# Optimization experiments

Hardware: AMD Instinct MI355X
Metric: run time of the kernel (lower is better)

## Reference

```python
import jax, jax.numpy as jnp
import numpy as np
import math

W = 64  # window_size == chunk_size == 64


def _windows(x, w):
    """x: [b, t, ...] -> [b, nb, 2w, ...]: for block j, concat(block j-1, block j).
    Block -1 is zero padding; its validity is handled by the attention mask."""
    b, t = x.shape[0], x.shape[1]
    nb = t // w
    pad = [(0, 0), (w, 0)] + [(0, 0)] * (x.ndim - 2)
    xp = jnp.pad(x, pad)                                   # [b, t+w, ...]
    xb = xp.reshape((b, nb + 1, w) + x.shape[2:])          # [b, nb+1, w, ...]
    return jnp.concatenate([xb[:, :-1], xb[:, 1:]], axis=2)  # [b, nb, 2w, ...]


def setup_inputs() -> dict:
    key = jax.random.key(0)
    k1, k2, k3 = jax.random.split(key, 3)
    b, t, h, d = 4, 4096, 16, 64
    return {
        "q": jax.random.normal(k1, (b, t, h, d), dtype=jnp.float32),
        "k": jax.random.normal(k2, (b, t, h, d), dtype=jnp.float32),
        "v": jax.random.normal(k3, (b, t, h, d), dtype=jnp.float32),
        "attn_mask": jnp.ones((b, t), dtype=jnp.int32),
    }


def reference(q, k, v, attn_mask):
    b, t, h, d = q.shape
    nb = t // W
    scale = 1.0 / math.sqrt(d)

    qb = q.reshape(b, nb, W, h, d)
    kw = _windows(k, W)                         # [b, nb, 2W, h, d]
    vw = _windows(v, W)                         # [b, nb, 2W, h, d]
    mw = _windows(attn_mask.astype(bool), W)    # [b, nb, 2W]

    # query local index i attends to key local index m iff 0 <= (i+W-m) < W
    i = jnp.arange(W)[:, None]
    m = jnp.arange(2 * W)[None, :]
    diff = i + W - m
    band = (diff >= 0) & (diff < W)             # [W, 2W]

    valid = band[None, None] & mw[:, :, None, :]          # [b, nb, W, 2W]

    scores = jnp.einsum('bnqhd,bnkhd->bnhqk', qb, kw) * scale  # [b,nb,h,W,2W]
    scores = jnp.where(valid[:, :, None], scores, jnp.float32(-1e9))
    attn = jax.nn.softmax(scores, axis=-1)
    attn = attn * valid[:, :, None].astype(attn.dtype)

    qm = attn_mask.astype(q.dtype).reshape(b, nb, W)      # query validity
    attn = attn * qm[:, :, None, :, None]

    out = jnp.einsum('bnhqk,bnkhd->bnqhd', attn, vw)      # [b,nb,W,h,d]
    out = out * qm[:, :, :, None, None]
    return out.reshape(b, t, h, d)
```

## Files before the change

kernel.cpp:

```cpp
#include <hip/hip_runtime.h>
#include <hip/hip_bf16.h>


#define TT 4096
#define HH 16
#define DD 64
#define WW 64
#define NBLK (TT / WW)

typedef __attribute__((ext_vector_type(8))) short bf16x8;
typedef __attribute__((ext_vector_type(4))) float f32x4;

static __device__ __forceinline__ ushort f2bf(float x) {
    return __builtin_bit_cast(unsigned short, __float2bfloat16(x));
}
static __device__ __forceinline__ uint pack2(float a, float b) {
    return (uint)f2bf(a) | ((uint)f2bf(b) << 16);
}

__global__ __launch_bounds__(256, 3)
void lca_fwd(const float* __restrict__ q, const float* __restrict__ k,
             const float* __restrict__ v, const int* __restrict__ am,
             float* __restrict__ out)
{
    const int jb = blockIdx.x;
    const int hi = blockIdx.y;
    const int bi = blockIdx.z;

    __shared__ union {
        struct { ushort Q[64][72]; ushort K[128][72]; } qk;
        ushort P[64][136];
    } u;
    __shared__ ushort sVt[64][136];
    __shared__ int    sKv[128];
    __shared__ int    sQv[64];

    const int tid = threadIdx.x;
    const size_t rowstride = (size_t)HH * DD;
    const size_t qbase = ((size_t)(bi * TT + jb * WW) * HH + hi) * DD;
    const long  kstart = (long)jb * WW - WW;

    if (tid < 128) {
        long tok = kstart + tid;
        sKv[tid] = (tok >= 0) && (am[(size_t)bi * TT + tok] != 0);
    } else if (tid < 192) {
        int r = tid - 128;
        sQv[r] = (am[(size_t)bi * TT + jb * WW + r] != 0);
    }

    float4 fq[4], fk[8], fv[8];
    #pragma unroll
    for (int p = 0; p < 4; ++p) {
        int idx = p * 256 + tid;
        int row = idx >> 4, c4 = (idx & 15) * 4;
        fq[p] = *(const float4*)(q + qbase + (size_t)row * rowstride + c4);
    }
    if (jb > 0) {
        #pragma unroll
        for (int p = 0; p < 8; ++p) {
            int idx = p * 256 + tid;
            int row = idx >> 4, c4 = (idx & 15) * 4;
            fk[p] = *(const float4*)(k + ((size_t)(bi * TT + kstart + row) * HH + hi) * DD + c4);
        }
        #pragma unroll
        for (int p = 0; p < 8; ++p) {
            int idx = p * 256 + tid;
            int row = idx >> 4, c4 = (idx & 15) * 4;
            fv[p] = *(const float4*)(v + ((size_t)(bi * TT + kstart + row) * HH + hi) * DD + c4);
        }
    } else {
        #pragma unroll
        for (int p = 0; p < 8; ++p) {
            float4 z = make_float4(0.f, 0.f, 0.f, 0.f);
            if (p >= 4) {
                int idx = p * 256 + tid;
                int row = idx >> 4, c4 = (idx & 15) * 4;
                z = *(const float4*)(k + ((size_t)(bi * TT + (row - 64)) * HH + hi) * DD + c4);
            }
            fk[p] = z;
        }
        #pragma unroll
        for (int p = 0; p < 8; ++p) {
            float4 z = make_float4(0.f, 0.f, 0.f, 0.f);
            if (p >= 4) {
                int idx = p * 256 + tid;
                int row = idx >> 4, c4 = (idx & 15) * 4;
                z = *(const float4*)(v + ((size_t)(bi * TT + (row - 64)) * HH + hi) * DD + c4);
            }
            fv[p] = z;
        }
    }

    #pragma unroll
    for (int p = 0; p < 4; ++p) {
        int idx = p * 256 + tid;
        int row = idx >> 4, c4 = (idx & 15) * 4;
        uint2 w; w.x = pack2(fq[p].x, fq[p].y); w.y = pack2(fq[p].z, fq[p].w);
        *(uint2*)(&u.qk.Q[row][c4]) = w;
    }
    #pragma unroll
    for (int p = 0; p < 8; ++p) {
        int idx = p * 256 + tid;
        int row = idx >> 4, c4 = (idx & 15) * 4;
        uint2 w; w.x = pack2(fk[p].x, fk[p].y); w.y = pack2(fk[p].z, fk[p].w);
        *(uint2*)(&u.qk.K[row][c4]) = w;
    }
    #pragma unroll
    for (int p = 0; p < 8; ++p) {
        int idx = p * 256 + tid;
        int row = idx >> 4, c4 = (idx & 15) * 4;
        sVt[c4 + 0][row] = f2bf(fv[p].x);
        sVt[c4 + 1][row] = f2bf(fv[p].y);
        sVt[c4 + 2][row] = f2bf(fv[p].z);
        sVt[c4 + 3][row] = f2bf(fv[p].w);
    }
    __syncthreads();

    const int wv = tid >> 6, lane = tid & 63;
    const int quad = lane >> 4, l15 = lane & 15;
    const int r0 = 16 * wv + quad * 4;

    bf16x8 aq0 = *(const bf16x8*)(&u.qk.Q[16 * wv + l15][quad * 8]);
    bf16x8 aq1 = *(const bf16x8*)(&u.qk.Q[16 * wv + l15][32 + quad * 8]);

    f32x4 acc[8];
    #pragma unroll
    for (int kt = 0; kt < 8; ++kt) {
        f32x4 a = {0.f, 0.f, 0.f, 0.f};
        bf16x8 b0 = *(const bf16x8*)(&u.qk.K[16 * kt + l15][quad * 8]);
        bf16x8 b1 = *(const bf16x8*)(&u.qk.K[16 * kt + l15][32 + quad * 8]);
        a = __builtin_amdgcn_mfma_f32_16x16x32_bf16(aq0, b0, a, 0, 0, 0);
        a = __builtin_amdgcn_mfma_f32_16x16x32_bf16(aq1, b1, a, 0, 0, 0);
        acc[kt] = a;
    }
    __syncthreads();

    const float NEG = -1.0e9f;
    float rmax[4] = {NEG, NEG, NEG, NEG};
    #pragma unroll
    for (int kt = 0; kt < 8; ++kt) {
        int c = 16 * kt + l15;
        int kvc = sKv[c];
        #pragma unroll
        for (int reg = 0; reg < 4; ++reg) {
            int r = r0 + reg;
            bool valid = (c > r) && (c <= r + WW) && kvc;
            float s = valid ? acc[kt][reg] : NEG;
            acc[kt][reg] = s;
            rmax[reg] = fmaxf(rmax[reg], s);
        }
    }
    #pragma unroll
    for (int reg = 0; reg < 4; ++reg) {
        #pragma unroll
        for (int m = 1; m <= 8; m <<= 1)
            rmax[reg] = fmaxf(rmax[reg], __shfl_xor(rmax[reg], m, 64));
    }

    const float CEXP = 0.125f * 1.44269504088896f;
    float rsum[4] = {0.f, 0.f, 0.f, 0.f};
    #pragma unroll
    for (int kt = 0; kt < 8; ++kt) {
        int c = 16 * kt + l15;
        #pragma unroll
        for (int reg = 0; reg < 4; ++reg) {
            float s = acc[kt][reg];
            float pex = (s > -1.0e8f) ? exp2f((s - rmax[reg]) * CEXP) : 0.f;
            rsum[reg] += pex;
            u.P[r0 + reg][c] = f2bf(pex);
        }
    }
    float rden[4];
    #pragma unroll
    for (int reg = 0; reg < 4; ++reg) {
        #pragma unroll
        for (int m = 1; m <= 8; m <<= 1)
            rsum[reg] += __shfl_xor(rsum[reg], m, 64);
        rden[reg] = (rsum[reg] > 0.f ? 1.f / rsum[reg] : 0.f)
                    * (float)sQv[r0 + reg];
    }

    bf16x8 ap[4];
    #pragma unroll
    for (int kc = 0; kc < 4; ++kc)
        ap[kc] = *(const bf16x8*)(&u.P[16 * wv + l15][kc * 32 + quad * 8]);

    #pragma unroll
    for (int nt = 0; nt < 4; ++nt) {
        f32x4 a = {0.f, 0.f, 0.f, 0.f};
        #pragma unroll
        for (int kc = 0; kc < 4; ++kc) {
            bf16x8 bv = *(const bf16x8*)(&sVt[16 * nt + l15][kc * 32 + quad * 8]);
            a = __builtin_amdgcn_mfma_f32_16x16x32_bf16(ap[kc], bv, a, 0, 0, 0);
        }
        #pragma unroll
        for (int reg = 0; reg < 4; ++reg)
            out[qbase + (size_t)(r0 + reg) * rowstride + 16 * nt + l15]
                = a[reg] * rden[reg];
    }
}

extern "C" void kernel_launch(void* const* d_in, const int* in_sizes, int n_in,
                              void* d_out, int out_size, void* d_ws, size_t ws_size,
                              hipStream_t stream) {
    const float* q  = (const float*)d_in[0];
    const float* k  = (const float*)d_in[1];
    const float* v  = (const float*)d_in[2];
    const int*   am = (const int*)d_in[3];
    float* out = (float*)d_out;

    const int b = in_sizes[3] / TT;
    dim3 grid(NBLK, HH, b);
    dim3 block(256);
    lca_fwd<<<grid, block, 0, stream>>>(q, k, v, am, out);
}
```

Before: 228.1 us.

## Swizzle LDS layouts, load Q directly to registers, ballot masks, reorder blocks

Replaces the padded shared-memory arrays with XOR-swizzled unpadded buffers for K, P and transposed V. Q is now loaded straight into MFMA operand registers instead of going through LDS. The attention-mask validity arrays are replaced by wavefront ballots. LDS use drops enough to allow raising the occupancy hint from 3 to 5. Block indices are also permuted so neighbouring chunks run on different workgroups, which may change L2 reuse of the overlapping K/V windows.

```diff
diff --git a/kernel.cpp b/kernel.cpp
--- a/kernel.cpp
+++ b/kernel.cpp
@@ -18,43 +18,34 @@
     return (uint)f2bf(a) | ((uint)f2bf(b) << 16);
 }
 
-__global__ __launch_bounds__(256, 3)
+__global__ __launch_bounds__(256, 5)
 void lca_fwd(const float* __restrict__ q, const float* __restrict__ k,
              const float* __restrict__ v, const int* __restrict__ am,
              float* __restrict__ out)
 {
-    const int jb = blockIdx.x;
+    const int jb = ((blockIdx.x & 7) << 3) | (blockIdx.x >> 3);
     const int hi = blockIdx.y;
     const int bi = blockIdx.z;
 
-    __shared__ union {
-        struct { ushort Q[64][72]; ushort K[128][72]; } qk;
-        ushort P[64][136];
-    } u;
-    __shared__ ushort sVt[64][136];
-    __shared__ int    sKv[128];
-    __shared__ int    sQv[64];
-
-    const int tid = threadIdx.x;
+    __shared__ ushort sKP[8192];
+    __shared__ ushort sVt[8192];
+
+    const int tid  = threadIdx.x;
+    const int wv   = tid >> 6, lane = tid & 63;
+    const int quad = lane >> 4, l15 = lane & 15;
+
     const size_t rowstride = (size_t)HH * DD;
     const size_t qbase = ((size_t)(bi * TT + jb * WW) * HH + hi) * DD;
     const long  kstart = (long)jb * WW - WW;
 
-    if (tid < 128) {
-        long tok = kstart + tid;
-        sKv[tid] = (tok >= 0) && (am[(size_t)bi * TT + tok] != 0);
-    } else if (tid < 192) {
-        int r = tid - 128;
-        sQv[r] = (am[(size_t)bi * TT + jb * WW + r] != 0);
-    }
-
-    float4 fq[4], fk[8], fv[8];
-    #pragma unroll
-    for (int p = 0; p < 4; ++p) {
-        int idx = p * 256 + tid;
-        int row = idx >> 4, c4 = (idx & 15) * 4;
-        fq[p] = *(const float4*)(q + qbase + (size_t)row * rowstride + c4);
-    }
+    const int* amb = am + (size_t)bi * TT;
+    long t0 = kstart + lane;
+    bool kv0 = (t0 >= 0) && (amb[t0] != 0);
+    bool qv  = (amb[jb * WW + lane] != 0);
+    unsigned long long kvm_lo = __ballot(kv0);
+    unsigned long long qvm    = __ballot(qv);
+
+    float4 fk[8], fv[8], fq[4];
     if (jb > 0) {
         #pragma unroll
         for (int p = 0; p < 8; ++p) {
@@ -90,47 +81,50 @@
             fv[p] = z;
         }
     }
-
-    #pragma unroll
-    for (int p = 0; p < 4; ++p) {
-        int idx = p * 256 + tid;
-        int row = idx >> 4, c4 = (idx & 15) * 4;
-        uint2 w; w.x = pack2(fq[p].x, fq[p].y); w.y = pack2(fq[p].z, fq[p].w);
-        *(uint2*)(&u.qk.Q[row][c4]) = w;
-    }
+    {
+        const float* qrow = q + qbase + (size_t)(16 * wv + l15) * rowstride;
+        fq[0] = *(const float4*)(qrow + quad * 8);
+        fq[1] = *(const float4*)(qrow + quad * 8 + 4);
+        fq[2] = *(const float4*)(qrow + 32 + quad * 8);
+        fq[3] = *(const float4*)(qrow + 32 + quad * 8 + 4);
+    }
+
     #pragma unroll
     for (int p = 0; p < 8; ++p) {
         int idx = p * 256 + tid;
         int row = idx >> 4, c4 = (idx & 15) * 4;
         uint2 w; w.x = pack2(fk[p].x, fk[p].y); w.y = pack2(fk[p].z, fk[p].w);
-        *(uint2*)(&u.qk.K[row][c4]) = w;
+        *(uint2*)(&sKP[row * 64 + (((c4 >> 3) ^ (row & 7)) << 3) + (c4 & 7)]) = w;
     }
     #pragma unroll
     for (int p = 0; p < 8; ++p) {
         int idx = p * 256 + tid;
         int row = idx >> 4, c4 = (idx & 15) * 4;
-        sVt[c4 + 0][row] = f2bf(fv[p].x);
-        sVt[c4 + 1][row] = f2bf(fv[p].y);
-        sVt[c4 + 2][row] = f2bf(fv[p].z);
-        sVt[c4 + 3][row] = f2bf(fv[p].w);
-    }
+        int u = row >> 3, k7 = row & 7;
+        sVt[(c4 + 0) * 128 + ((u ^ ((c4 + 0) & 15)) << 3) + k7] = f2bf(fv[p].x);
+        sVt[(c4 + 1) * 128 + ((u ^ ((c4 + 1) & 15)) << 3) + k7] = f2bf(fv[p].y);
+        sVt[(c4 + 2) * 128 + ((u ^ ((c4 + 2) & 15)) << 3) + k7] = f2bf(fv[p].z);
+        sVt[(c4 + 3) * 128 + ((u ^ ((c4 + 3) & 15)) << 3) + k7] = f2bf(fv[p].w);
+    }
+    union { bf16x8 v8; uint u[4]; } A0, A1;
+    A0.u[0] = pack2(fq[0].x, fq[0].y); A0.u[1] = pack2(fq[0].z, fq[0].w);
+    A0.u[2] = pack2(fq[1].x, fq[1].y); A0.u[3] = pack2(fq[1].z, fq[1].w);
+    A1.u[0] = pack2(fq[2].x, fq[2].y); A1.u[1] = pack2(fq[2].z, fq[2].w);
+    A1.u[2] = pack2(fq[3].x, fq[3].y); A1.u[3] = pack2(fq[3].z, fq[3].w);
     __syncthreads();
 
-    const int wv = tid >> 6, lane = tid & 63;
-    const int quad = lane >> 4, l15 = lane & 15;
-    const int r0 = 16 * wv + quad * 4;
-
-    bf16x8 aq0 = *(const bf16x8*)(&u.qk.Q[16 * wv + l15][quad * 8]);
-    bf16x8 aq1 = *(const bf16x8*)(&u.qk.Q[16 * wv + l15][32 + quad * 8]);
+    const int r0 = 16 * wv + 4 * quad;
+    const int r7 = l15 & 7;
 
     f32x4 acc[8];
     #pragma unroll
     for (int kt = 0; kt < 8; ++kt) {
         f32x4 a = {0.f, 0.f, 0.f, 0.f};
-        bf16x8 b0 = *(const bf16x8*)(&u.qk.K[16 * kt + l15][quad * 8]);
-        bf16x8 b1 = *(const bf16x8*)(&u.qk.K[16 * kt + l15][32 + quad * 8]);
-        a = __builtin_amdgcn_mfma_f32_16x16x32_bf16(aq0, b0, a, 0, 0, 0);
-        a = __builtin_amdgcn_mfma_f32_16x16x32_bf16(aq1, b1, a, 0, 0, 0);
+        const ushort* kr = &sKP[(16 * kt + l15) * 64];
+        bf16x8 b0 = *(const bf16x8*)(kr + ((quad ^ r7) << 3));
+        bf16x8 b1 = *(const bf16x8*)(kr + (((4 + quad) ^ r7) << 3));
+        a = __builtin_amdgcn_mfma_f32_16x16x32_bf16(A0.v8, b0, a, 0, 0, 0);
+        a = __builtin_amdgcn_mfma_f32_16x16x32_bf16(A1.v8, b1, a, 0, 0, 0);
         acc[kt] = a;
     }
     __syncthreads();
@@ -140,7 +134,8 @@
     #pragma unroll
     for (int kt = 0; kt < 8; ++kt) {
         int c = 16 * kt + l15;
-        int kvc = sKv[c];
+        unsigned long long km = (kt < 4) ? kvm_lo : qvm;
+        int kvc = (int)((km >> (c & 63)) & 1ull);
         #pragma unroll
         for (int reg = 0; reg < 4; ++reg) {
             int r = r0 + reg;
@@ -158,16 +153,18 @@
     }
 
     const float CEXP = 0.125f * 1.44269504088896f;
+    const int l7 = l15 & 7, h3 = l15 >> 3;
     float rsum[4] = {0.f, 0.f, 0.f, 0.f};
     #pragma unroll
     for (int kt = 0; kt < 8; ++kt) {
-        int c = 16 * kt + l15;
+        int cu = 2 * kt + h3;
         #pragma unroll
         for (int reg = 0; reg < 4; ++reg) {
             float s = acc[kt][reg];
             float pex = (s > -1.0e8f) ? exp2f((s - rmax[reg]) * CEXP) : 0.f;
             rsum[reg] += pex;
-            u.P[r0 + reg][c] = f2bf(pex);
+            int r = r0 + reg;
+            sKP[r * 128 + ((cu ^ (4 * quad + reg)) << 3) + l7] = f2bf(pex);
         }
     }
     float rden[4];
@@ -177,20 +174,22 @@
         for (int m = 1; m <= 8; m <<= 1)
             rsum[reg] += __shfl_xor(rsum[reg], m, 64);
         rden[reg] = (rsum[reg] > 0.f ? 1.f / rsum[reg] : 0.f)
-                    * (float)sQv[r0 + reg];
+                    * (float)((qvm >> (r0 + reg)) & 1ull);
     }
 
     bf16x8 ap[4];
+    const ushort* pr = &sKP[(16 * wv + l15) * 128];
     #pragma unroll
     for (int kc = 0; kc < 4; ++kc)
-        ap[kc] = *(const bf16x8*)(&u.P[16 * wv + l15][kc * 32 + quad * 8]);
+        ap[kc] = *(const bf16x8*)(pr + (((4 * kc + quad) ^ l15) << 3));
 
     #pragma unroll
     for (int nt = 0; nt < 4; ++nt) {
         f32x4 a = {0.f, 0.f, 0.f, 0.f};
+        const ushort* vr = &sVt[(16 * nt + l15) * 128];
         #pragma unroll
         for (int kc = 0; kc < 4; ++kc) {
-            bf16x8 bv = *(const bf16x8*)(&sVt[16 * nt + l15][kc * 32 + quad * 8]);
+            bf16x8 bv = *(const bf16x8*)(vr + (((4 * kc + quad) ^ l15) << 3));
             a = __builtin_amdgcn_mfma_f32_16x16x32_bf16(ap[kc], bv, a, 0, 0, 0);
         }
         #pragma unroll
```

After: 229.6 us. About the same (+0.7%).
